# Kernel tuning notes

Hardware: AMD Instinct MI355X
Metric: run time of the kernel (lower is better)

## Reference

```python
import jax, jax.numpy as jnp
import numpy as np

HIDDEN = 4096
N_HEAD = 16
HEAD_DIM = HIDDEN // N_HEAD          # 256
ROTARY_DIM = HEAD_DIM // 2           # 128 (partial rotary, GPT-J config)
ROPE_BASE = 10000.0
B, S = 4, 1024


def _apply_rope(x, position_ids):
    # x: [B, S, H, D]; rotate first ROTARY_DIM dims, NeoX/rotate-half style.
    rot, pas = x[..., :ROTARY_DIM], x[..., ROTARY_DIM:]
    inv_freq = 1.0 / (ROPE_BASE ** (jnp.arange(0, ROTARY_DIM, 2, dtype=jnp.float32) / ROTARY_DIM))
    ang = position_ids.astype(jnp.float32)[..., None] * inv_freq      # [B, S, R/2]
    cos = jnp.cos(ang)[:, :, None, :]                                  # [B, S, 1, R/2]
    sin = jnp.sin(ang)[:, :, None, :]
    x1, x2 = rot[..., : ROTARY_DIM // 2], rot[..., ROTARY_DIM // 2:]
    rot_out = jnp.concatenate([x1 * cos - x2 * sin, x2 * cos + x1 * sin], axis=-1)
    return jnp.concatenate([rot_out, pas], axis=-1)


def setup_inputs() -> dict:
    key = jax.random.key(0)
    k1, k2, k3 = jax.random.split(key, 3)
    hidden_states = jax.random.normal(k1, (B, S, HIDDEN), dtype=jnp.float32)
    w_qkv = jax.random.normal(k2, (HIDDEN, 3 * HIDDEN), dtype=jnp.float32) * (HIDDEN ** -0.5)
    w_out = jax.random.normal(k3, (HIDDEN, HIDDEN), dtype=jnp.float32) * (HIDDEN ** -0.5)
    position_ids = jnp.broadcast_to(jnp.arange(S, dtype=jnp.int32)[None, :], (B, S))
    return {"position_ids": position_ids, "hidden_states": hidden_states,
            "w_qkv": w_qkv, "w_out": w_out}


def reference(position_ids, hidden_states, w_qkv, w_out):
    qkv = hidden_states @ w_qkv                       # [B, S, 3H]
    q, k, v = jnp.split(qkv, 3, axis=-1)
    q = q.reshape(B, S, N_HEAD, HEAD_DIM)
    k = k.reshape(B, S, N_HEAD, HEAD_DIM)
    v = v.reshape(B, S, N_HEAD, HEAD_DIM)
    q = _apply_rope(q, position_ids)
    k = _apply_rope(k, position_ids)
    scale = HEAD_DIM ** -0.5
    scores = jnp.einsum('bqhd,bkhd->bhqk', q, k) * scale   # [B, H, S, S]
    causal = jnp.tril(jnp.ones((S, S), dtype=bool))
    scores = jnp.where(causal[None, None], scores, jnp.finfo(scores.dtype).min)
    probs = jax.nn.softmax(scores, axis=-1)
    attn = jnp.einsum('bhqk,bkhd->bqhd', probs, v).reshape(B, S, HIDDEN)
    return attn @ w_out
```

## Files before the change

### kernel.cpp

```cpp
#include <hip/hip_runtime.h>
#include <cstdint>

#define HID  4096
#define NHD  16
#define HDIM 256
#define SEQ  1024
#define BB   4
#define N3   12288
#define TOK  4096

typedef unsigned short u16;
typedef __bf16 bf16x8 __attribute__((ext_vector_type(8)));
typedef float  f32x4  __attribute__((ext_vector_type(4)));
typedef float  f32x16 __attribute__((ext_vector_type(16)));

__device__ __forceinline__ u16 f2b(float f) {
    unsigned u = __builtin_bit_cast(unsigned, f);
    u += 0x7fffu + ((u >> 16) & 1u);
    return (u16)(u >> 16);
}
__device__ __forceinline__ float b2f(u16 v) {
    unsigned u = ((unsigned)v) << 16;
    return __builtin_bit_cast(float, u);
}

typedef __attribute__((address_space(3))) unsigned       lds_u32;
typedef const __attribute__((address_space(1))) unsigned glb_u32;
__device__ __forceinline__ void async16(const void* g, void* l) {
    __builtin_amdgcn_global_load_lds((glb_u32*)g, (lds_u32*)l, 16, 0, 0);
}

__global__ __launch_bounds__(256) void cast_bf16(const float4* __restrict__ in,
                                                 uint4* __restrict__ out, int n8) {
    int i = blockIdx.x * 256 + threadIdx.x;
    if (i >= n8) return;
    float4 a = in[2 * i], b = in[2 * i + 1];
    union { u16 h[8]; uint4 v; } o;
    o.h[0] = f2b(a.x); o.h[1] = f2b(a.y); o.h[2] = f2b(a.z); o.h[3] = f2b(a.w);
    o.h[4] = f2b(b.x); o.h[5] = f2b(b.y); o.h[6] = f2b(b.z); o.h[7] = f2b(b.w);
    out[i] = o.v;
}

__global__ __launch_bounds__(256) void tcast(const float* __restrict__ in,
                                             u16* __restrict__ out, int R, int C) {
    __shared__ u16 sT[64 * 80];
    const int c0 = blockIdx.x * 64, r0 = blockIdx.y * 64;
    const int t = threadIdx.x;
    const int rr = t >> 4, cc = (t & 15) * 4;
    for (int rnd = 0; rnd < 4; rnd++) {
        int r = rnd * 16 + rr;
        float4 v = *(const float4*)(in + (size_t)(r0 + r) * C + c0 + cc);
        sT[(cc + 0) * 80 + r] = f2b(v.x);
        sT[(cc + 1) * 80 + r] = f2b(v.y);
        sT[(cc + 2) * 80 + r] = f2b(v.z);
        sT[(cc + 3) * 80 + r] = f2b(v.w);
    }
    __syncthreads();
    const int orow = t >> 2, oc = (t & 3) * 16;
    u16* dst = out + (size_t)(c0 + orow) * R + r0 + oc;
    *(uint4*)dst       = *(uint4*)&sT[orow * 80 + oc];
    *(uint4*)(dst + 8) = *(uint4*)&sT[orow * 80 + oc + 8];
}

template <bool OUT_BF16>
__global__ __launch_bounds__(512, 2) void gemm256(const u16* __restrict__ A,
                                                  const u16* __restrict__ Bt,
                                                  void* __restrict__ Cout,
                                                  int M, int N, int K) {
    __shared__ alignas(16) u16 lds[65536];
    const int t = threadIdx.x;
    const int lane = t & 63, w = t >> 6;
    const int wm = w >> 2, wn = w & 3;
    const int fm = lane & 15, g = lane >> 4;

    const int nwg = (int)gridDim.x;
    const int cpx = nwg >> 3;
    const int swz = (((int)blockIdx.x) & 7) * cpx + (((int)blockIdx.x) >> 3);
    const int gm = M >> 8;
    const int mblk = swz % gm, nblk = swz / gm;
    const int m0 = mblk << 8, n0 = nblk << 8;

    const int srow = t >> 2;
    const int schk = ((t & 3) ^ (srow & 3) ^ ((srow >> 2) & 2)) * 8;
    const u16* gA = A  + (size_t)(m0 + srow) * K + schk;
    const u16* gB = Bt + (size_t)(n0 + srow) * K + schk;
    const size_t hstep = (size_t)128 * K;
    const int ldst = t * 8;

    const int cxor = (g ^ (fm & 3) ^ ((fm >> 2) & 2)) * 8;
    const int aoff = (wm * 128 + fm) * 32 + cxor;
    const int boff = 16384 + (wn * 64 + fm) * 32 + cxor;

    f32x4 acc[8][4];
#pragma unroll
    for (int i = 0; i < 8; i++)
#pragma unroll
        for (int j = 0; j < 4; j++) acc[i][j] = f32x4{0.f, 0.f, 0.f, 0.f};

    const int nk = K >> 6;

#define STG_A(BO, KT, KS) do { \
    const u16* s_ = gA + (size_t)(KT) * 64 + (KS) * 32; \
    async16(s_,         &lds[(BO) + (KS) * 8192 + ldst]); \
    async16(s_ + hstep, &lds[(BO) + (KS) * 8192 + 4096 + ldst]); } while (0)
#define STG_B(BO, KT, KS) do { \
    const u16* s_ = gB + (size_t)(KT) * 64 + (KS) * 32; \
    async16(s_,         &lds[(BO) + 16384 + (KS) * 8192 + ldst]); \
    async16(s_ + hstep, &lds[(BO) + 16384 + (KS) * 8192 + 4096 + ldst]); } while (0)

    bf16x8 a0[4], a1[4], bfr[4];

#define LD_A0(BO, KS) { _Pragma("unroll") for (int m_ = 0; m_ < 4; m_++) \
    a0[m_] = *(const bf16x8*)&lds[(BO) + (KS) * 8192 + aoff + m_ * 512]; }
#define LD_A1(BO, KS) { _Pragma("unroll") for (int m_ = 0; m_ < 4; m_++) \
    a1[m_] = *(const bf16x8*)&lds[(BO) + (KS) * 8192 + 2048 + aoff + m_ * 512]; }
#define LD_B(BO, KS) { _Pragma("unroll") for (int n_ = 0; n_ < 4; n_++) \
    bfr[n_] = *(const bf16x8*)&lds[(BO) + (KS) * 8192 + boff + n_ * 512]; }
#define MM(AR, MO) { _Pragma("unroll") for (int m_ = 0; m_ < 4; m_++) \
    _Pragma("unroll") for (int n_ = 0; n_ < 4; n_++) \
    acc[(MO) + m_][n_] = __builtin_amdgcn_mfma_f32_16x16x32_bf16(AR[m_], bfr[n_], acc[(MO) + m_][n_], 0, 0, 0); }
#define BARX __builtin_amdgcn_s_barrier()
#define LGKM0 asm volatile("s_waitcnt lgkmcnt(0)" ::: "memory")
#define VM(N_) asm volatile("s_waitcnt vmcnt(" #N_ ")" ::: "memory")
#define PHASE_MID BARX; LGKM0; __builtin_amdgcn_s_setprio(1)
#define PHASE_END __builtin_amdgcn_s_setprio(0); BARX

    STG_A(0, 0, 0); STG_B(0, 0, 0); STG_A(0, 0, 1); STG_B(0, 0, 1);
    VM(4); BARX;

#pragma unroll 1
    for (int kt = 0; kt < nk - 1; kt++) {
        const int bo = (kt & 1) << 15, nb = bo ^ 32768;
        LD_A0(bo, 0); LD_B(bo, 0);
        STG_A(nb, kt + 1, 0);
        PHASE_MID; MM(a0, 0); PHASE_END;
        LD_A1(bo, 0);
        STG_B(nb, kt + 1, 0);
        VM(4);
        PHASE_MID; MM(a1, 4); PHASE_END;
        LD_A0(bo, 1); LD_B(bo, 1);
        STG_A(nb, kt + 1, 1);
        PHASE_MID; MM(a0, 0); PHASE_END;
        LD_A1(bo, 1);
        STG_B(nb, kt + 1, 1);
        VM(4);
        PHASE_MID; MM(a1, 4); PHASE_END;
    }
    {
        const int bo = ((nk - 1) & 1) << 15;
        LD_A0(bo, 0); LD_B(bo, 0);
        PHASE_MID; MM(a0, 0); PHASE_END;
        LD_A1(bo, 0);
        VM(0);
        PHASE_MID; MM(a1, 4); PHASE_END;
        LD_A0(bo, 1); LD_B(bo, 1);
        PHASE_MID; MM(a0, 0); PHASE_END;
        LD_A1(bo, 1);
        PHASE_MID; MM(a1, 4); PHASE_END;
    }

    const int crow0 = m0 + wm * 128 + g * 4;
    const int ccol = n0 + wn * 64 + fm;
#pragma unroll
    for (int mi = 0; mi < 8; mi++)
#pragma unroll
        for (int r = 0; r < 4; r++) {
            const size_t row = (size_t)(crow0 + mi * 16 + r);
            if (OUT_BF16) {
                u16* p = (u16*)Cout + row * N + ccol;
#pragma unroll
                for (int n_ = 0; n_ < 4; n_++) p[n_ * 16] = f2b(acc[mi][n_][r]);
            } else {
                float* p = (float*)Cout + row * N + ccol;
#pragma unroll
                for (int n_ = 0; n_ < 4; n_++) p[n_ * 16] = acc[mi][n_][r];
            }
        }
#undef STG_A
#undef STG_B
#undef LD_A0
#undef LD_A1
#undef LD_B
#undef MM
#undef BARX
#undef LGKM0
#undef VM
#undef PHASE_MID
#undef PHASE_END
}

__global__ __launch_bounds__(256) void rope_relayout(const int* __restrict__ pos_ids,
                                                     const u16* __restrict__ qkv,
                                                     u16* __restrict__ Qo,
                                                     u16* __restrict__ Ko,
                                                     u16* __restrict__ VTo) {
    __shared__ u16 sV[64 * 256];
    const int st = blockIdx.x, h = blockIdx.y, b = blockIdx.z;
    const int t = threadIdx.x;
    const int sbase = st * 64;

    {
        const u16* vbase = qkv + (size_t)(b * SEQ + sbase) * N3 + 2 * HID + h * HDIM;
        const int dcol = (t & 31) * 8;
        const int tokoff = t >> 5;
#pragma unroll
        for (int r = 0; r < 4; r++)
#pragma unroll
            for (int s8 = 0; s8 < 8; s8++) {
                int tok = r * 16 + s8 * 2 + tokoff;
                async16(vbase + (size_t)tok * N3 + dcol, &sV[r * 4096 + s8 * 512 + t * 8]);
            }
    }

    const int tok = t & 63, part = t >> 6;
    const int s = sbase + tok;
    const int pos = pos_ids[b * SEQ + s];
    const int isK = part >> 1, isPass = part & 1;
    const u16* src = qkv + (size_t)(b * SEQ + s) * N3 + isK * HID + h * HDIM + isPass * 128;
    u16* dst = (isK ? Ko : Qo) + ((size_t)((b * NHD + h) * SEQ + s)) * HDIM + isPass * 128;
    if (!isPass) {
        const float fpos = (float)pos;
#pragma unroll
        for (int c = 0; c < 8; c++) {
            bf16x8 xa = *(const bf16x8*)(src + c * 8);
            bf16x8 xb = *(const bf16x8*)(src + 64 + c * 8);
            union { u16 h[8]; uint4 v; } o1, o2;
#pragma unroll
            for (int j = 0; j < 8; j++) {
                int i = c * 8 + j;
                float invf = __expf((float)i * -0.14391156831212787f);
                float ang = fpos * invf;
                float sn, cs;
                __sincosf(ang, &sn, &cs);
                float x1 = (float)xa[j], x2 = (float)xb[j];
                o1.h[j] = f2b(x1 * cs - x2 * sn);
                o2.h[j] = f2b(x2 * cs + x1 * sn);
            }
            *(uint4*)(dst + c * 8)      = o1.v;
            *(uint4*)(dst + 64 + c * 8) = o2.v;
        }
    } else {
        const uint4* s4 = (const uint4*)src;
        uint4* d4 = (uint4*)dst;
#pragma unroll
        for (int c = 0; c < 16; c++) d4[c] = s4[c];
    }

    asm volatile("s_waitcnt vmcnt(0)" ::: "memory");
    __syncthreads();

    u16* vt = VTo + ((size_t)((b * NHD + h) * HDIM + t)) * SEQ + sbase;
#pragma unroll
    for (int g = 0; g < 8; g++) {
        union { u16 h[8]; uint4 v; } o;
#pragma unroll
        for (int j = 0; j < 8; j++) o.h[j] = sV[(g * 8 + j) * 256 + t];
        *(uint4*)(vt + g * 8) = o.v;
    }
}

__global__ __launch_bounds__(256) void attn_fwd(const u16* __restrict__ Q,
                                                const u16* __restrict__ K,
                                                const u16* __restrict__ VT,
                                                u16* __restrict__ attnO) {
    __shared__ u16 sK[32 * 256];
    __shared__ u16 sVT[256 * 32];
    __shared__ u16 sP[4 * 16 * 32];
    const int qt = (int)gridDim.x - 1 - (int)blockIdx.x;
    const int h = blockIdx.y, b = blockIdx.z;
    const int t = threadIdx.x, lane = t & 63, w = t >> 6;
    const int fm = lane & 15, g = lane >> 4, fk = g * 8;
    const int qbase = qt * 64;
    const size_t head = ((size_t)(b * NHD + h)) * SEQ * HDIM;
    const u16* qptr = Q + head + (size_t)(qbase + w * 16 + fm) * HDIM;
    bf16x8 qf[8];
#pragma unroll
    for (int kk = 0; kk < 8; kk++) qf[kk] = *(const bf16x8*)(qptr + kk * 32 + fk);
    const f32x4 z = {0.f, 0.f, 0.f, 0.f};
    f32x4 O[16];
#pragma unroll
    for (int n = 0; n < 16; n++) O[n] = z;
    float mrow[4] = {-1e30f, -1e30f, -1e30f, -1e30f};
    float lrow[4] = {0.f, 0.f, 0.f, 0.f};
    const int nkt = qt * 2 + 2;
    const u16* kbaseP = K + head;
    const u16* vtbase = VT + head;
    const int qg_base = qbase + w * 16 + g * 4;

    for (int kb = 0; kb < nkt; kb++) {
        {
            const int krow = t >> 5;
            const int dcol = ((t & 31) ^ krow) * 8;
#pragma unroll
            for (int r = 0; r < 4; r++)
                async16(kbaseP + (size_t)(kb * 32 + r * 8 + krow) * HDIM + dcol,
                        &sK[r * 2048 + t * 8]);
            const int drow = t >> 2;
            const int scol = (((t & 3) ^ (drow & 3))) * 8;
#pragma unroll
            for (int r = 0; r < 4; r++)
                async16(vtbase + (size_t)(r * 64 + drow) * SEQ + kb * 32 + scol,
                        &sVT[r * 2048 + t * 8]);
        }
        asm volatile("s_waitcnt vmcnt(0)" ::: "memory");
        __syncthreads();

        f32x4 sc0 = z, sc1 = z;
#pragma unroll
        for (int kk = 0; kk < 8; kk++) {
            const int p = ((kk * 4 + g) ^ (fm & 7)) * 8;
            bf16x8 kf0 = *(const bf16x8*)&sK[fm * 256 + p];
            bf16x8 kf1 = *(const bf16x8*)&sK[(16 + fm) * 256 + p];
            sc0 = __builtin_amdgcn_mfma_f32_16x16x32_bf16(qf[kk], kf0, sc0, 0, 0, 0);
            sc1 = __builtin_amdgcn_mfma_f32_16x16x32_bf16(qf[kk], kf1, sc1, 0, 0, 0);
        }
        const int kg0 = kb * 32 + fm, kg1 = kg0 + 16;
        float alpha[4];
#pragma unroll
        for (int j = 0; j < 4; j++) {
            const int qg = qg_base + j;
            float s0 = (kg0 <= qg) ? sc0[j] * 0.0625f : -1e30f;
            float s1 = (kg1 <= qg) ? sc1[j] * 0.0625f : -1e30f;
            float mx = fmaxf(s0, s1);
            mx = fmaxf(mx, __shfl_xor(mx, 1, 64));
            mx = fmaxf(mx, __shfl_xor(mx, 2, 64));
            mx = fmaxf(mx, __shfl_xor(mx, 4, 64));
            mx = fmaxf(mx, __shfl_xor(mx, 8, 64));
            const float mn = fmaxf(mrow[j], mx);
            alpha[j] = __expf(mrow[j] - mn);
            mrow[j] = mn;
            float p0 = __expf(s0 - mn);
            float p1 = __expf(s1 - mn);
            float rs = p0 + p1;
            rs += __shfl_xor(rs, 1, 64);
            rs += __shfl_xor(rs, 2, 64);
            rs += __shfl_xor(rs, 4, 64);
            rs += __shfl_xor(rs, 8, 64);
            lrow[j] = lrow[j] * alpha[j] + rs;
            const int r = g * 4 + j;
            sP[w * 512 + r * 32 + fm]      = f2b(p0);
            sP[w * 512 + r * 32 + 16 + fm] = f2b(p1);
        }
#pragma unroll
        for (int n = 0; n < 16; n++) {
            O[n][0] *= alpha[0]; O[n][1] *= alpha[1];
            O[n][2] *= alpha[2]; O[n][3] *= alpha[3];
        }
        bf16x8 pf = *(const bf16x8*)&sP[w * 512 + fm * 32 + fk];
#pragma unroll
        for (int n = 0; n < 16; n++) {
            const int d = n * 16 + fm;
            bf16x8 vf = *(const bf16x8*)&sVT[d * 32 + ((g ^ (fm & 3)) << 3)];
            O[n] = __builtin_amdgcn_mfma_f32_16x16x32_bf16(pf, vf, O[n], 0, 0, 0);
        }
        __syncthreads();
    }
#pragma unroll
    for (int j = 0; j < 4; j++) {
        const int r = g * 4 + j;
        const float inv = 1.0f / lrow[j];
        u16* orow = attnO + (size_t)(b * SEQ + qbase + w * 16 + r) * HID + h * HDIM;
#pragma unroll
        for (int n = 0; n < 16; n++)
            orow[n * 16 + fm] = f2b(O[n][j] * inv);
    }
}

extern "C" void kernel_launch(void* const* d_in, const int* in_sizes, int n_in,
                              void* d_out, int out_size, void* d_ws, size_t ws_size,
                              hipStream_t stream) {
    (void)in_sizes; (void)n_in; (void)out_size; (void)ws_size;
    const int*   pos    = (const int*)d_in[0];
    const float* hidden = (const float*)d_in[1];
    const float* wqkv   = (const float*)d_in[2];
    const float* wout   = (const float*)d_in[3];
    float* out = (float*)d_out;
    char* ws = (char*)d_ws;

    u16* hiddenB = (u16*)ws;
    u16* wqkvT   = (u16*)(ws + (size_t)33554432);
    u16* woutT   = (u16*)(ws + (size_t)134217728);
    u16* qkv     = (u16*)(ws + (size_t)167772160);
    u16* Qb    = wqkvT;
    u16* Kb    = wqkvT + 16777216;
    u16* VTb   = wqkvT + 33554432;
    u16* attnB = qkv;

    cast_bf16<<<dim3(TOK * HID / 8 / 256), 256, 0, stream>>>(
        (const float4*)hidden, (uint4*)hiddenB, TOK * HID / 8);
    tcast<<<dim3(N3 / 64, HID / 64), 256, 0, stream>>>(wqkv, wqkvT, HID, N3);
    tcast<<<dim3(HID / 64, HID / 64), 256, 0, stream>>>(wout, woutT, HID, HID);
    gemm256<true><<<dim3((TOK / 256) * (N3 / 256)), 512, 0, stream>>>(
        hiddenB, wqkvT, qkv, TOK, N3, HID);
    rope_relayout<<<dim3(SEQ / 64, NHD, BB), 256, 0, stream>>>(pos, qkv, Qb, Kb, VTb);
    attn_fwd<<<dim3(SEQ / 64, NHD, BB), 256, 0, stream>>>(Qb, Kb, VTb, attnB);
    gemm256<false><<<dim3((TOK / 256) * (HID / 256)), 512, 0, stream>>>(
        attnB, woutT, out, TOK, HID, HID);
}
```

Baseline: 1.210 ms.

## Double-buffer K/V tiles in attention, precompute RoPE table, skip unneeded rescales

The attention kernel now double-buffers K and V^T tiles in shared memory, prefetching the next tile while the current one is computed. This replaces the serial load-wait-compute pattern. It also raises wave priority around the MFMA loops and skips the O-accumulator rescale when no row max grew in the wave. Separately, RoPE cos/sin values are computed once per (batch, token, freq) into a table in the workspace (reusing the hiddenB region after the QKV GEMM), so the 16 heads no longer each recompute them. This costs one extra small launch plus table reads, and doubles the attention kernel's shared memory, which may lower occupancy.

```diff
diff --git a/kernel.cpp b/kernel.cpp
--- a/kernel.cpp
+++ b/kernel.cpp
@@ -189,7 +189,18 @@
 #undef PHASE_END
 }
 
-__global__ __launch_bounds__(256) void rope_relayout(const int* __restrict__ pos_ids,
+__global__ __launch_bounds__(256) void rope_tab(const int* __restrict__ pos_ids,
+                                                float2* __restrict__ tab) {
+    const int idx = blockIdx.x * 256 + threadIdx.x;
+    const int bs = idx >> 6, i = idx & 63;
+    const float invf = __expf((float)i * -0.14391156831212787f);
+    const float ang = (float)pos_ids[bs] * invf;
+    float sn, cs;
+    __sincosf(ang, &sn, &cs);
+    tab[idx] = make_float2(cs, sn);
+}
+
+__global__ __launch_bounds__(256) void rope_relayout(const float2* __restrict__ tab,
                                                      const u16* __restrict__ qkv,
                                                      u16* __restrict__ Qo,
                                                      u16* __restrict__ Ko,
@@ -214,12 +225,11 @@
 
     const int tok = t & 63, part = t >> 6;
     const int s = sbase + tok;
-    const int pos = pos_ids[b * SEQ + s];
     const int isK = part >> 1, isPass = part & 1;
     const u16* src = qkv + (size_t)(b * SEQ + s) * N3 + isK * HID + h * HDIM + isPass * 128;
     u16* dst = (isK ? Ko : Qo) + ((size_t)((b * NHD + h) * SEQ + s)) * HDIM + isPass * 128;
     if (!isPass) {
-        const float fpos = (float)pos;
+        const float2* trow = tab + ((size_t)(b * SEQ + s) << 6);
 #pragma unroll
         for (int c = 0; c < 8; c++) {
             bf16x8 xa = *(const bf16x8*)(src + c * 8);
@@ -227,11 +237,8 @@
             union { u16 h[8]; uint4 v; } o1, o2;
 #pragma unroll
             for (int j = 0; j < 8; j++) {
-                int i = c * 8 + j;
-                float invf = __expf((float)i * -0.14391156831212787f);
-                float ang = fpos * invf;
-                float sn, cs;
-                __sincosf(ang, &sn, &cs);
+                float2 t2 = trow[c * 8 + j];
+                const float cs = t2.x, sn = t2.y;
                 float x1 = (float)xa[j], x2 = (float)xb[j];
                 o1.h[j] = f2b(x1 * cs - x2 * sn);
                 o2.h[j] = f2b(x2 * cs + x1 * sn);
@@ -263,8 +270,8 @@
                                                 const u16* __restrict__ K,
                                                 const u16* __restrict__ VT,
                                                 u16* __restrict__ attnO) {
-    __shared__ u16 sK[32 * 256];
-    __shared__ u16 sVT[256 * 32];
+    __shared__ u16 sK[2][32 * 256];
+    __shared__ u16 sVT[2][32 * 256];
     __shared__ u16 sP[4 * 16 * 32];
     const int qt = (int)gridDim.x - 1 - (int)blockIdx.x;
     const int h = blockIdx.y, b = blockIdx.z;
@@ -287,35 +294,41 @@
     const u16* vtbase = VT + head;
     const int qg_base = qbase + w * 16 + g * 4;
 
+    const int krow = t >> 5;
+    const int dcol = ((t & 31) ^ krow) * 8;
+    const int drow = t >> 2;
+    const int scol = ((t & 3) ^ (drow & 3)) * 8;
+
+#define STAGE_KV(BUF, KB) do { \
+    _Pragma("unroll") for (int r_ = 0; r_ < 4; r_++) \
+        async16(kbaseP + (size_t)((KB) * 32 + r_ * 8 + krow) * HDIM + dcol, \
+                &sK[BUF][r_ * 2048 + t * 8]); \
+    _Pragma("unroll") for (int r_ = 0; r_ < 4; r_++) \
+        async16(vtbase + (size_t)(r_ * 64 + drow) * SEQ + (KB) * 32 + scol, \
+                &sVT[BUF][r_ * 2048 + t * 8]); } while (0)
+
+    STAGE_KV(0, 0);
+    asm volatile("s_waitcnt vmcnt(0)" ::: "memory");
+    __syncthreads();
+
     for (int kb = 0; kb < nkt; kb++) {
-        {
-            const int krow = t >> 5;
-            const int dcol = ((t & 31) ^ krow) * 8;
-#pragma unroll
-            for (int r = 0; r < 4; r++)
-                async16(kbaseP + (size_t)(kb * 32 + r * 8 + krow) * HDIM + dcol,
-                        &sK[r * 2048 + t * 8]);
-            const int drow = t >> 2;
-            const int scol = (((t & 3) ^ (drow & 3))) * 8;
-#pragma unroll
-            for (int r = 0; r < 4; r++)
-                async16(vtbase + (size_t)(r * 64 + drow) * SEQ + kb * 32 + scol,
-                        &sVT[r * 2048 + t * 8]);
-        }
-        asm volatile("s_waitcnt vmcnt(0)" ::: "memory");
-        __syncthreads();
+        const int cur = kb & 1;
+        if (kb + 1 < nkt) STAGE_KV(cur ^ 1, kb + 1);
 
         f32x4 sc0 = z, sc1 = z;
+        __builtin_amdgcn_s_setprio(1);
 #pragma unroll
         for (int kk = 0; kk < 8; kk++) {
             const int p = ((kk * 4 + g) ^ (fm & 7)) * 8;
-            bf16x8 kf0 = *(const bf16x8*)&sK[fm * 256 + p];
-            bf16x8 kf1 = *(const bf16x8*)&sK[(16 + fm) * 256 + p];
+            bf16x8 kf0 = *(const bf16x8*)&sK[cur][fm * 256 + p];
+            bf16x8 kf1 = *(const bf16x8*)&sK[cur][(16 + fm) * 256 + p];
             sc0 = __builtin_amdgcn_mfma_f32_16x16x32_bf16(qf[kk], kf0, sc0, 0, 0, 0);
             sc1 = __builtin_amdgcn_mfma_f32_16x16x32_bf16(qf[kk], kf1, sc1, 0, 0, 0);
         }
+        __builtin_amdgcn_s_setprio(0);
         const int kg0 = kb * 32 + fm, kg1 = kg0 + 16;
         float alpha[4];
+        bool grow = false;
 #pragma unroll
         for (int j = 0; j < 4; j++) {
             const int qg = qg_base + j;
@@ -327,6 +340,7 @@
             mx = fmaxf(mx, __shfl_xor(mx, 4, 64));
             mx = fmaxf(mx, __shfl_xor(mx, 8, 64));
             const float mn = fmaxf(mrow[j], mx);
+            grow = grow || (mn > mrow[j]);
             alpha[j] = __expf(mrow[j] - mn);
             mrow[j] = mn;
             float p0 = __expf(s0 - mn);
@@ -341,20 +355,26 @@
             sP[w * 512 + r * 32 + fm]      = f2b(p0);
             sP[w * 512 + r * 32 + 16 + fm] = f2b(p1);
         }
-#pragma unroll
-        for (int n = 0; n < 16; n++) {
-            O[n][0] *= alpha[0]; O[n][1] *= alpha[1];
-            O[n][2] *= alpha[2]; O[n][3] *= alpha[3];
+        if (__any(grow)) {
+#pragma unroll
+            for (int n = 0; n < 16; n++) {
+                O[n][0] *= alpha[0]; O[n][1] *= alpha[1];
+                O[n][2] *= alpha[2]; O[n][3] *= alpha[3];
+            }
         }
         bf16x8 pf = *(const bf16x8*)&sP[w * 512 + fm * 32 + fk];
+        __builtin_amdgcn_s_setprio(1);
 #pragma unroll
         for (int n = 0; n < 16; n++) {
             const int d = n * 16 + fm;
-            bf16x8 vf = *(const bf16x8*)&sVT[d * 32 + ((g ^ (fm & 3)) << 3)];
+            bf16x8 vf = *(const bf16x8*)&sVT[cur][d * 32 + ((g ^ (fm & 3)) << 3)];
             O[n] = __builtin_amdgcn_mfma_f32_16x16x32_bf16(pf, vf, O[n], 0, 0, 0);
         }
+        __builtin_amdgcn_s_setprio(0);
+        asm volatile("s_waitcnt vmcnt(0)" ::: "memory");
         __syncthreads();
     }
+#undef STAGE_KV
 #pragma unroll
     for (int j = 0; j < 4; j++) {
         const int r = g * 4 + j;
@@ -385,6 +405,7 @@
     u16* Kb    = wqkvT + 16777216;
     u16* VTb   = wqkvT + 33554432;
     u16* attnB = qkv;
+    float2* tabF = (float2*)ws;
 
     cast_bf16<<<dim3(TOK * HID / 8 / 256), 256, 0, stream>>>(
         (const float4*)hidden, (uint4*)hiddenB, TOK * HID / 8);
@@ -392,7 +413,8 @@
     tcast<<<dim3(HID / 64, HID / 64), 256, 0, stream>>>(wout, woutT, HID, HID);
     gemm256<true><<<dim3((TOK / 256) * (N3 / 256)), 512, 0, stream>>>(
         hiddenB, wqkvT, qkv, TOK, N3, HID);
-    rope_relayout<<<dim3(SEQ / 64, NHD, BB), 256, 0, stream>>>(pos, qkv, Qb, Kb, VTb);
+    rope_tab<<<dim3(BB * SEQ * 64 / 256), 256, 0, stream>>>(pos, tabF);
+    rope_relayout<<<dim3(SEQ / 64, NHD, BB), 256, 0, stream>>>(tabF, qkv, Qb, Kb, VTb);
     attn_fwd<<<dim3(SEQ / 64, NHD, BB), 256, 0, stream>>>(Qb, Kb, VTb, attnB);
     gemm256<false><<<dim3((TOK / 256) * (HID / 256)), 512, 0, stream>>>(
         attnB, woutT, out, TOK, HID, HID);
```

Result: faster. 1.099 ms (-9.2%).
